# Kernel tuning notes

Measured on AMD Instinct MI355X. Metric: run time of the kernel, lower is better.

Reference implementation:

```python
import jax, jax.numpy as jnp
import numpy as np

N, E, B = 100000, 160000, 4096
F_NODE, F_EDGE, H, DEPTH = 133, 14, 512, 5


def setup_inputs() -> dict:
    key = jax.random.key(0)
    ks = jax.random.split(key, 12)
    P = E // 2
    src = jax.random.randint(ks[0], (P,), 0, N)
    dst = jax.random.randint(ks[1], (P,), 0, N)
    # interleave so edge 2k = (src,dst) and 2k+1 = (dst,src); reverse of e is e^1
    row = jnp.stack([src, dst], axis=1).reshape(-1)
    col = jnp.stack([dst, src], axis=1).reshape(-1)
    edge_index = jnp.stack([row, col], axis=0)
    x = jax.random.normal(ks[2], (N, F_NODE), jnp.float32)
    edge_attr = jax.random.normal(ks[3], (E, F_EDGE), jnp.float32)
    batch = jnp.sort(jax.random.randint(ks[4], (N,), 0, B))
    s = 0.05
    return dict(
        x=x, edge_attr=edge_attr, edge_index=edge_index, batch=batch,
        W_init=jax.random.normal(ks[5], (F_NODE + F_EDGE, H), jnp.float32) * s,
        b_init=jnp.zeros((H,), jnp.float32),
        W_conv=jax.random.normal(ks[6], (DEPTH, H, H), jnp.float32) * s,
        b_conv=jnp.zeros((DEPTH, H), jnp.float32),
        W_e2n=jax.random.normal(ks[7], (F_NODE + H, H), jnp.float32) * s,
        b_e2n=jnp.zeros((H,), jnp.float32),
        W_ffn1=jax.random.normal(ks[8], (H, H), jnp.float32) * s,
        b_ffn1=jnp.zeros((H,), jnp.float32),
        W_ffn2=jax.random.normal(ks[9], (H, 1), jnp.float32) * s,
        b_ffn2=jnp.zeros((1,), jnp.float32),
    )


def _dmpnn_conv(h, row, col, rev, W, b):
    # node aggregation: sum incoming edge messages at each destination node
    a = jax.ops.segment_sum(h, col, num_segments=N)          # [N, H]
    # new edge message for (i->j): agg at i minus reverse-edge message (j->i)
    msg = a[row] - h[rev]                                    # [E, H]
    return a, msg @ W + b


def reference(x, edge_attr, edge_index, batch, W_init, b_init, W_conv, b_conv,
              W_e2n, b_e2n, W_ffn1, b_ffn1, W_ffn2, b_ffn2):
    row, col = edge_index[0], edge_index[1]
    rev = jnp.arange(E) ^ 1
    # edge_init: relu(Linear(cat([x[row], edge_attr])))
    h0 = jax.nn.relu(jnp.concatenate([x[row], edge_attr], axis=1) @ W_init + b_init)
    h = h0
    for l in range(DEPTH):
        _, h = _dmpnn_conv(h, row, col, rev, W_conv[l], b_conv[l])
        h = jax.nn.relu(h + h0)  # residual to h0, relu (dropout=0, eval mode)
    # final conv reuses last layer (l == DEPTH-1 as in the torch loop variable)
    s_node, _ = _dmpnn_conv(h, row, col, rev, W_conv[DEPTH - 1], b_conv[DEPTH - 1])
    q = jnp.concatenate([x, s_node], axis=1)                 # [N, F_NODE+H]
    hn = jax.nn.relu(q @ W_e2n + b_e2n)                      # [N, H]
    pooled = jax.ops.segment_sum(hn, batch, num_segments=B)  # global_add_pool [B, H]
    out = jax.nn.relu(pooled @ W_ffn1 + b_ffn1) @ W_ffn2 + b_ffn2
    return out.squeeze(-1)                                   # [B]
```

## Files before the change

### kernel.cpp

```cpp
#include <hip/hip_runtime.h>

typedef _Float16 f16;
typedef _Float16 f16x2 __attribute__((ext_vector_type(2)));
typedef _Float16 f16x4 __attribute__((ext_vector_type(4)));
typedef _Float16 f16x8 __attribute__((ext_vector_type(8)));
typedef float f32x4 __attribute__((ext_vector_type(4)));

#define NN 100000
#define NE 160000
#define NB 4096
#define HD 512

#define O_H8    0UL
#define O_SCE   81920000UL
#define O_SHR   87040000UL
#define O_WT    141440000UL
#define O_OFF   145437696UL
#define O_EID   145837712UL
#define WS_NEEDED 146477712UL
#define V_POOL  0UL
#define V_PH    8388608UL
#define V_T1    12582912UL
#define V_CNT   16777216UL
#define V_FILL  17177232UL
#define V_BSUM  17577248UL

__global__ void zero16(ulong2* __restrict__ p, long n) {
  long i = (long)blockIdx.x * 256 + threadIdx.x;
  if (i < n) p[i] = ulong2{0UL, 0UL};
}
__global__ void diag(float* __restrict__ out, int n, float v) {
  int i = blockIdx.x * 256 + threadIdx.x;
  if (i < n) out[i] = v;
}

__global__ void transcast(const float* __restrict__ src, f16* __restrict__ dst,
                          int Kreal, int Kpad) {
  int id = blockIdx.x * 256 + threadIdx.x;
  if (id >= 512 * Kpad) return;
  int n = id / Kpad, k = id % Kpad;
  dst[((k >> 5) * 512 + n) * 32 + (k & 31)] =
      (k < Kreal) ? (f16)src[(size_t)k * 512 + n] : (f16)0.f;
}

__global__ void countK(const int* __restrict__ col, int* __restrict__ cnt) {
  int e = blockIdx.x * 256 + threadIdx.x;
  if (e < NE) atomicAdd(&cnt[col[e]], 1);
}
__global__ __launch_bounds__(1024) void scanA(const int* __restrict__ cnt,
                                              int* __restrict__ incl, int* __restrict__ bsum) {
  __shared__ int s[1024];
  int i = blockIdx.x * 1024 + threadIdx.x;
  s[threadIdx.x] = (i < NN) ? cnt[i] : 0;
  __syncthreads();
  for (int d = 1; d < 1024; d <<= 1) {
    int t = (threadIdx.x >= d) ? s[threadIdx.x - d] : 0;
    __syncthreads();
    s[threadIdx.x] += t;
    __syncthreads();
  }
  if (i < NN) incl[i] = s[threadIdx.x];
  if (threadIdx.x == 1023) bsum[blockIdx.x] = s[1023];
}
__global__ void scanB(int* bsum, int nb) {
  if (threadIdx.x == 0 && blockIdx.x == 0) {
    int run = 0;
    for (int i = 0; i < nb; ++i) { int t = bsum[i]; bsum[i] = run; run += t; }
  }
}
__global__ __launch_bounds__(1024) void scanC(const int* __restrict__ cnt,
                                              int* __restrict__ incl_fill,
                                              const int* __restrict__ bsum,
                                              int* __restrict__ off) {
  int i = blockIdx.x * 1024 + threadIdx.x;
  if (i >= NN) return;
  int g = incl_fill[i] + bsum[blockIdx.x];
  off[i + 1] = g;
  incl_fill[i] = g - cnt[i];
  if (i == 0) off[0] = 0;
}
__global__ void scatterK(const int* __restrict__ col, int* __restrict__ fill,
                         int* __restrict__ eid) {
  int e = blockIdx.x * 256 + threadIdx.x;
  if (e >= NE) return;
  int p = atomicAdd(&fill[col[e]], 1);
  eid[p] = e;
}

template<int C0>
__global__ __launch_bounds__(256, 4)
void msgk(const char* __restrict__ z8, const float* __restrict__ sce,
          const int* __restrict__ off, const int* __restrict__ eid,
          char* __restrict__ msgq, float* __restrict__ scm) {
  int tid = threadIdx.x, wid = tid >> 6, lane = tid & 63;
  int n = blockIdx.x * 4 + wid;
  int s0 = off[n], s1 = off[n + 1];
  int cnt = s1 - s0;
  int g = lane >> 4;
  float a[4] = {0.f, 0.f, 0.f, 0.f};
  int ec[8]; unsigned uc[8]; float scc[8];
  #pragma unroll
  for (int i = 0; i < 8; ++i) {
    if (i < cnt) {
      int e = eid[s0 + i];
      ec[i] = e;
      scc[i] = sce[e * 8 + (C0 >> 6) + g];
      uc[i] = *reinterpret_cast<const unsigned*>(z8 + (size_t)e * 512 + C0 + lane * 4);
      #pragma unroll
      for (int b = 0; b < 4; ++b)
        a[b] += (float)(char)((uc[i] >> (8 * b)) & 0xff) * scc[i];
    }
  }
  for (int p = s0 + 8; p < s1; ++p) {
    int e = eid[p];
    float sc = sce[e * 8 + (C0 >> 6) + g];
    unsigned u = *reinterpret_cast<const unsigned*>(z8 + (size_t)e * 512 + C0 + lane * 4);
    #pragma unroll
    for (int b = 0; b < 4; ++b)
      a[b] += (float)(char)((u >> (8 * b)) & 0xff) * sc;
  }
  #pragma unroll
  for (int i = 0; i < 8; ++i) {
    if (i < cnt) {
      int f = ec[i] ^ 1;
      float mv[4]; float m = 0.f;
      #pragma unroll
      for (int b = 0; b < 4; ++b) {
        mv[b] = a[b] - (float)(char)((uc[i] >> (8 * b)) & 0xff) * scc[i];
        m = fmaxf(m, fabsf(mv[b]));
      }
      #pragma unroll
      for (int d = 1; d < 16; d <<= 1) m = fmaxf(m, __shfl_xor(m, d));
      float s2 = (m > 0.f) ? m / 127.f : 1.f;
      if ((lane & 15) == 0) scm[f * 4 + g] = s2;
      unsigned q = 0;
      #pragma unroll
      for (int b = 0; b < 4; ++b) {
        int qi = __float2int_rn(mv[b] / s2);
        qi = min(127, max(-127, qi));
        q |= ((unsigned)(unsigned char)(char)qi) << (8 * b);
      }
      *reinterpret_cast<unsigned*>(msgq + (size_t)f * 256 + lane * 4) = q;
    }
  }
  for (int p = s0 + 8; p < s1; ++p) {
    int e = eid[p];
    int f = e ^ 1;
    float sc = sce[e * 8 + (C0 >> 6) + g];
    unsigned u = *reinterpret_cast<const unsigned*>(z8 + (size_t)e * 512 + C0 + lane * 4);
    float mv[4]; float m = 0.f;
    #pragma unroll
    for (int b = 0; b < 4; ++b) {
      mv[b] = a[b] - (float)(char)((u >> (8 * b)) & 0xff) * sc;
      m = fmaxf(m, fabsf(mv[b]));
    }
    #pragma unroll
    for (int d = 1; d < 16; d <<= 1) m = fmaxf(m, __shfl_xor(m, d));
    float s2 = (m > 0.f) ? m / 127.f : 1.f;
    if ((lane & 15) == 0) scm[f * 4 + g] = s2;
    unsigned q = 0;
    #pragma unroll
    for (int b = 0; b < 4; ++b) {
      int qi = __float2int_rn(mv[b] / s2);
      qi = min(127, max(-127, qi));
      q |= ((unsigned)(unsigned char)(char)qi) << (8 * b);
    }
    *reinterpret_cast<unsigned*>(msgq + (size_t)f * 256 + lane * 4) = q;
  }
}

__global__ __launch_bounds__(256, 4)
void tker(const char* __restrict__ h8, const float* __restrict__ sce,
          const int* __restrict__ off, const int* __restrict__ eid,
          char* __restrict__ nb8, float* __restrict__ scn) {
  int tid = threadIdx.x, wid = tid >> 6, lane = tid & 63;
  int n = blockIdx.x * 4 + wid;
  int s0 = off[n], s1 = off[n + 1];
  int g = lane >> 3;
  float a[8] = {0.f,0.f,0.f,0.f,0.f,0.f,0.f,0.f};
  for (int p = s0; p < s1; ++p) {
    int e = eid[p];
    float sc = sce[e * 8 + g];
    uint2 u = *reinterpret_cast<const uint2*>(h8 + (size_t)e * 512 + lane * 8);
    #pragma unroll
    for (int b = 0; b < 4; ++b) {
      a[b]     += (float)((u.x >> (8 * b)) & 0xff) * sc;
      a[4 + b] += (float)((u.y >> (8 * b)) & 0xff) * sc;
    }
  }
  float m = 0.f;
  #pragma unroll
  for (int j = 0; j < 8; ++j) m = fmaxf(m, a[j]);
  #pragma unroll
  for (int d = 1; d < 8; d <<= 1) m = fmaxf(m, __shfl_xor(m, d));
  float s2 = (m > 0.f) ? m / 255.f : 1.f;
  if ((lane & 7) == 0) scn[n * 8 + g] = s2;
  unsigned lo = 0, hi = 0;
  #pragma unroll
  for (int b = 0; b < 4; ++b) {
    int q0 = __float2int_rn(a[b] / s2);     q0 = min(255, max(0, q0));
    int q1 = __float2int_rn(a[4 + b] / s2); q1 = min(255, max(0, q1));
    lo |= ((unsigned)q0) << (8 * b);
    hi |= ((unsigned)q1) << (8 * b);
  }
  *reinterpret_cast<uint2*>(nb8 + (size_t)n * 512 + lane * 8) = uint2{lo, hi};
}

static __device__ __forceinline__ void stageB512(const f16* __restrict__ wsrc,
                                                 f16* __restrict__ Bs, int tid) {
  #pragma unroll
  for (int j = 0; j < 4; ++j) {
    int u = tid * 4 + j;
    *reinterpret_cast<f16x8*>(&Bs[(u >> 2) * 40 + (u & 3) * 8]) =
        *reinterpret_cast<const f16x8*>(&wsrc[u * 8]);
  }
}
template<int AS>
static __device__ __forceinline__ void mstep8(const f16* __restrict__ As,
                                              const f16* __restrict__ Bs,
                                              f32x4 acc[2][8], int wm, int wn,
                                              int fr, int fg, int ko) {
  f16x8 af[2];
  #pragma unroll
  for (int mf = 0; mf < 2; ++mf)
    af[mf] = *reinterpret_cast<const f16x8*>(&As[(wm + mf * 16 + fr) * AS + ko + fg * 8]);
  #pragma unroll
  for (int nf = 0; nf < 8; ++nf) {
    f16x8 bf = *reinterpret_cast<const f16x8*>(&Bs[(wn + nf * 16 + fr) * 40 + fg * 8]);
    #pragma unroll
    for (int mf = 0; mf < 2; ++mf)
      acc[mf][nf] = __builtin_amdgcn_mfma_f32_16x16x32_f16(af[mf], bf, acc[mf][nf], 0, 0, 0);
  }
}

static __device__ __forceinline__ void loadBfrag(const f16* __restrict__ wp,
                                                 f16x8 bf[8], int wn, int fr, int fg) {
  #pragma unroll
  for (int nf = 0; nf < 8; ++nf)
    bf[nf] = *reinterpret_cast<const f16x8*>(&wp[(size_t)(wn + nf * 16 + fr) * 32 + fg * 8]);
}

static __device__ __forceinline__ f16x2 pkfma(f16x2 a, f16x2 b, f16x2 c) {
  f16x2 r;
  asm("v_pk_fma_f16 %0, %1, %2, %3" : "=v"(r) : "v"(a), "v"(b), "v"(c));
  return r;
}

static __device__ __forceinline__ void stageXrow(const float* __restrict__ xr,
                                                 f16* __restrict__ dstRow, int s) {
  #pragma unroll
  for (int j = 0; j < 4; ++j) {
    float v[4];
    __builtin_memcpy(v, xr + 4 * s + 32 * j, 16);
    f16 t4[4];
    #pragma unroll
    for (int b = 0; b < 4; ++b) t4[b] = (f16)v[b];
    *reinterpret_cast<f16x4*>(&dstRow[4 * s + 32 * j]) = *reinterpret_cast<f16x4*>(t4);
  }
  if (s < 5) dstRow[128 + s] = (f16)xr[128 + s];
}

__global__ __launch_bounds__(512, 4)
void zk(char* __restrict__ h8, float* __restrict__ sce, const f16* __restrict__ wst) {
  __shared__ f16 Af[64 * 264];
  __shared__ f16 Bs[512 * 40];
  const int tid = threadIdx.x, lane = tid & 63, wid = tid >> 6;
  const int fr = lane & 15, fg = lane >> 4;
  const int wm = (wid >> 2) * 32, wn = (wid & 3) * 128;
  const int e0 = blockIdx.x * 64;
  const int sr = tid >> 3;
  const int sc8 = tid & 7;

  auto stageA = [&](int phase) {
    const int kb = phase * 256 + sc8 * 32;
    float sa = sce[(size_t)(e0 + sr) * 8 + (kb >> 6)];
    const f16 sh = (f16)sa;
    const f16 bh = (f16)(-1024.f * sa);
    f16x2 s2; s2[0] = sh; s2[1] = sh;
    f16x2 b2; b2[0] = bh; b2[1] = bh;
    const int4* src = reinterpret_cast<const int4*>(h8 + (size_t)(e0 + sr) * 512 + kb);
    f16* dst = &Af[sr * 264 + sc8 * 32];
    #pragma unroll
    for (int j = 0; j < 2; ++j) {
      int4 w = src[j];
      unsigned vv[4] = {(unsigned)w.x, (unsigned)w.y, (unsigned)w.z, (unsigned)w.w};
      #pragma unroll
      for (int q = 0; q < 2; ++q) {
        unsigned p0 = __builtin_amdgcn_perm(0x64646464u, vv[2*q],     0x05010400u);
        unsigned p1 = __builtin_amdgcn_perm(0x64646464u, vv[2*q],     0x05030402u);
        unsigned p2 = __builtin_amdgcn_perm(0x64646464u, vv[2*q + 1], 0x05010400u);
        unsigned p3 = __builtin_amdgcn_perm(0x64646464u, vv[2*q + 1], 0x05030402u);
        uint4 o;
        o.x = __builtin_bit_cast(unsigned, pkfma(__builtin_bit_cast(f16x2, p0), s2, b2));
        o.y = __builtin_bit_cast(unsigned, pkfma(__builtin_bit_cast(f16x2, p1), s2, b2));
        o.z = __builtin_bit_cast(unsigned, pkfma(__builtin_bit_cast(f16x2, p2), s2, b2));
        o.w = __builtin_bit_cast(unsigned, pkfma(__builtin_bit_cast(f16x2, p3), s2, b2));
        *reinterpret_cast<uint4*>(dst + j * 16 + q * 8) = o;
      }
    }
  };

  stageA(0);
  f32x4 acc[2][8] = {};
  for (int step = 0; step < 16; ++step) {
    if (step == 8) stageA(1);
    stageB512(wst + (size_t)step * 16384, Bs, tid);
    __syncthreads();
    const int ko = (step & 7) * 32;
    f16x8 af[2];
    #pragma unroll
    for (int mf = 0; mf < 2; ++mf)
      af[mf] = *reinterpret_cast<const f16x8*>(&Af[(wm + mf * 16 + fr) * 264 + ko + fg * 8]);
    #pragma unroll
    for (int nf = 0; nf < 8; ++nf) {
      f16x8 bf = *reinterpret_cast<const f16x8*>(&Bs[(wn + nf * 16 + fr) * 40 + fg * 8]);
      #pragma unroll
      for (int mf = 0; mf < 2; ++mf)
        acc[mf][nf] = __builtin_amdgcn_mfma_f32_16x16x32_f16(af[mf], bf, acc[mf][nf], 0, 0, 0);
    }
    __syncthreads();
  }
  float scA[2][4], scB[2][4];
  #pragma unroll
  for (int mf = 0; mf < 2; ++mf)
    #pragma unroll
    for (int i = 0; i < 4; ++i) {
      float mA = 0.f, mB = 0.f;
      #pragma unroll
      for (int nf = 0; nf < 4; ++nf) mA = fmaxf(mA, fabsf(acc[mf][nf][i]));
      #pragma unroll
      for (int nf = 4; nf < 8; ++nf) mB = fmaxf(mB, fabsf(acc[mf][nf][i]));
      #pragma unroll
      for (int d = 1; d < 16; d <<= 1) {
        mA = fmaxf(mA, __shfl_xor(mA, d));
        mB = fmaxf(mB, __shfl_xor(mB, d));
      }
      scA[mf][i] = (mA > 0.f) ? mA / 127.f : 1.f;
      scB[mf][i] = (mB > 0.f) ? mB / 127.f : 1.f;
      if (fr == 0) {
        int r = wm + mf * 16 + fg * 4 + i;
        sce[(size_t)(e0 + r) * 8 + (wn >> 6)]     = scA[mf][i];
        sce[(size_t)(e0 + r) * 8 + (wn >> 6) + 1] = scB[mf][i];
      }
    }
  char* q8 = (char*)&Bs[0];
  #pragma unroll
  for (int mf = 0; mf < 2; ++mf)
    #pragma unroll
    for (int nf = 0; nf < 8; ++nf) {
      int c = wn + nf * 16 + fr;
      #pragma unroll
      for (int i = 0; i < 4; ++i) {
        int r = wm + mf * 16 + fg * 4 + i;
        float s = (nf < 4) ? scA[mf][i] : scB[mf][i];
        int q = __float2int_rn(acc[mf][nf][i] / s);
        q8[r * 512 + c] = (char)min(127, max(-127, q));
      }
    }
  __syncthreads();
  { int4* dst = reinterpret_cast<int4*>(h8 + (size_t)e0 * 512);
    const int4* s4 = reinterpret_cast<const int4*>(q8);
    #pragma unroll
    for (int j = 0; j < 4; ++j) dst[tid * 4 + j] = s4[tid * 4 + j]; }
}

template<int MODE>
__global__ __launch_bounds__(512, 2)
void convup(const float* __restrict__ x, const float* __restrict__ ea,
            const int* __restrict__ row, const f16* __restrict__ wi,
            const float* __restrict__ bi, const float* __restrict__ bc,
            char* __restrict__ h8, float* __restrict__ sce,
            const char* __restrict__ msgq, const float* __restrict__ scm,
            int c0) {
  __shared__ f16 As[64 * 168];
  __shared__ f16 Bs[2][256 * 40];
  __shared__ char m8s[64 * 256];
  __shared__ float scmL[64 * 4];
  const int tid = threadIdx.x, lane = tid & 63, wid = tid >> 6;
  const int fr = lane & 15, fg = lane >> 4;
  const int wm = (wid >> 2) * 32, wn = (wid & 3) * 64;
  const int e0 = blockIdx.x * 64;

  {
    int r = tid >> 3, s = tid & 7;
    int rid = row[e0 + r];
    stageXrow(x + (size_t)rid * 133, &As[r * 168], s);
    if (s < 7) {
      float2 e2 = *reinterpret_cast<const float2*>(ea + (size_t)(e0 + r) * 14 + 2 * s);
      As[r * 168 + 133 + 2 * s]     = (f16)e2.x;
      As[r * 168 + 133 + 2 * s + 1] = (f16)e2.y;
    }
    for (int k = 147 + s; k < 160; k += 8) As[r * 168 + k] = (f16)0.f;
    if (MODE == 1) {
      const int4* ms = reinterpret_cast<const int4*>(msgq + (size_t)(e0 + r) * 256 + s * 32);
      int4* md = reinterpret_cast<int4*>(m8s + r * 256 + s * 32);
      md[0] = ms[0]; md[1] = ms[1];
      if (s < 4) scmL[r * 4 + s] = scm[(size_t)(e0 + r) * 4 + s];
    }
  }
  {
    #pragma unroll
    for (int j = 0; j < 2; ++j) {
      int u = tid * 2 + j;
      *reinterpret_cast<f16x8*>(&Bs[0][(u >> 2) * 40 + (u & 3) * 8]) =
          *reinterpret_cast<const f16x8*>(&wi[(size_t)c0 * 32 + (size_t)u * 8]);
    }
  }
  __syncthreads();
  f32x4 acc[2][4] = {};
  for (int step = 0; step < 5; ++step) {
    const int cur = step & 1;
    f16x8 pf[2];
    if (step < 4) {
      const f16* wsrc = wi + (size_t)(step + 1) * 16384 + (size_t)c0 * 32;
      #pragma unroll
      for (int j = 0; j < 2; ++j)
        pf[j] = *reinterpret_cast<const f16x8*>(&wsrc[(size_t)(tid * 2 + j) * 8]);
    }
    f16x8 af[2];
    #pragma unroll
    for (int mf = 0; mf < 2; ++mf)
      af[mf] = *reinterpret_cast<const f16x8*>(&As[(wm + mf * 16 + fr) * 168 + step * 32 + fg * 8]);
    #pragma unroll
    for (int nf = 0; nf < 4; ++nf) {
      f16x8 bf = *reinterpret_cast<const f16x8*>(&Bs[cur][(wn + nf * 16 + fr) * 40 + fg * 8]);
      #pragma unroll
      for (int mf = 0; mf < 2; ++mf)
        acc[mf][nf] = __builtin_amdgcn_mfma_f32_16x16x32_f16(af[mf], bf, acc[mf][nf], 0, 0, 0);
    }
    if (step < 4) {
      #pragma unroll
      for (int j = 0; j < 2; ++j) {
        int u = tid * 2 + j;
        *reinterpret_cast<f16x8*>(&Bs[cur ^ 1][(u >> 2) * 40 + (u & 3) * 8]) = pf[j];
      }
    }
    __syncthreads();
  }
  #pragma unroll
  for (int nf = 0; nf < 4; ++nf) {
    int cl = wn + nf * 16 + fr;
    int cg = c0 + cl;
    float bi_ = bi[cg];
    float bc_ = (MODE == 1) ? bc[cg] : 0.f;
    #pragma unroll
    for (int mf = 0; mf < 2; ++mf)
      #pragma unroll
      for (int i = 0; i < 4; ++i) {
        int r = wm + mf * 16 + fg * 4 + i;
        float v = fmaxf(acc[mf][nf][i] + bi_, 0.f);
        if (MODE == 1) {
          float mv = (float)(char)m8s[r * 256 + cl] * scmL[r * 4 + (cl >> 6)];
          v = fmaxf(v + bc_ + mv, 0.f);
        }
        acc[mf][nf][i] = v;
      }
  }
  float sc_[2][4];
  #pragma unroll
  for (int mf = 0; mf < 2; ++mf)
    #pragma unroll
    for (int i = 0; i < 4; ++i) {
      float m = 0.f;
      #pragma unroll
      for (int nf = 0; nf < 4; ++nf) m = fmaxf(m, acc[mf][nf][i]);
      #pragma unroll
      for (int d = 1; d < 16; d <<= 1) m = fmaxf(m, __shfl_xor(m, d));
      sc_[mf][i] = (m > 0.f) ? m / 255.f : 1.f;
      if (fr == 0)
        sce[(size_t)(e0 + wm + mf * 16 + fg * 4 + i) * 8 + (c0 >> 6) + (wn >> 6)] = sc_[mf][i];
    }
  __syncthreads();
  #pragma unroll
  for (int mf = 0; mf < 2; ++mf)
    #pragma unroll
    for (int nf = 0; nf < 4; ++nf) {
      int cl = wn + nf * 16 + fr;
      #pragma unroll
      for (int i = 0; i < 4; ++i) {
        int r = wm + mf * 16 + fg * 4 + i;
        int q = __float2int_rn(acc[mf][nf][i] / sc_[mf][i]);
        m8s[r * 256 + cl] = (char)(unsigned char)min(255, max(0, q));
      }
    }
  __syncthreads();
  { int r = tid >> 3, s = tid & 7;
    int4* dst = reinterpret_cast<int4*>(h8 + (size_t)(e0 + r) * 512 + c0 + s * 32);
    const int4* sp = reinterpret_cast<const int4*>(m8s + r * 256 + s * 32);
    dst[0] = sp[0]; dst[1] = sp[1]; }
}

__global__ __launch_bounds__(512, 4)
void e2n(const float* __restrict__ x, const char* __restrict__ nb8,
         const float* __restrict__ scn, const f16* __restrict__ wex,
         const f16* __restrict__ wes, const float* __restrict__ be,
         const int* __restrict__ batch, float* __restrict__ pooled) {
  __shared__ f16 As[64 * 520];
  __shared__ int bat[64];
  const int tid = threadIdx.x, lane = tid & 63, wid = tid >> 6;
  const int fr = lane & 15, fg = lane >> 4;
  const int wm = (wid >> 2) * 32, wn = (wid & 3) * 128;
  const int n0 = blockIdx.x * 64;
  if (tid < 64) { int nn = n0 + tid; bat[tid] = (nn < NN) ? batch[nn] : 0; }
  {
    int r = tid >> 3, s = tid & 7;
    int nid = min(n0 + r, NN - 1);
    stageXrow(x + (size_t)nid * 133, &As[r * 168], s);
    for (int k = 133 + s; k < 160; k += 8) As[r * 168 + k] = (f16)0.f;
  }
  __syncthreads();
  f32x4 acc[2][8] = {};
  for (int step = 0; step < 5; ++step) {
    f16x8 bf[8];
    loadBfrag(wex + (size_t)step * 16384, bf, wn, fr, fg);
    f16x8 af[2];
    #pragma unroll
    for (int mf = 0; mf < 2; ++mf)
      af[mf] = *reinterpret_cast<const f16x8*>(&As[(wm + mf * 16 + fr) * 168 + step * 32 + fg * 8]);
    #pragma unroll
    for (int nf = 0; nf < 8; ++nf)
      #pragma unroll
      for (int mf = 0; mf < 2; ++mf)
        acc[mf][nf] = __builtin_amdgcn_mfma_f32_16x16x32_f16(af[mf], bf[nf], acc[mf][nf], 0, 0, 0);
  }
  __syncthreads();
  {
    int r = tid >> 3, s = tid & 7, kb = s * 64;
    int nid = min(n0 + r, NN - 1);
    float sc = scn[(size_t)nid * 8 + s];
    const int4* src = reinterpret_cast<const int4*>(nb8 + (size_t)nid * 512 + kb);
    #pragma unroll
    for (int j = 0; j < 4; ++j) {
      int4 w = src[j];
      unsigned vv[4] = {(unsigned)w.x, (unsigned)w.y, (unsigned)w.z, (unsigned)w.w};
      f16 tmp[16];
      #pragma unroll
      for (int q = 0; q < 4; ++q)
        #pragma unroll
        for (int b = 0; b < 4; ++b)
          tmp[q * 4 + b] = (f16)((float)((vv[q] >> (8 * b)) & 0xff) * sc);
      *reinterpret_cast<f16x8*>(&As[r * 520 + kb + j * 16])     = *reinterpret_cast<f16x8*>(&tmp[0]);
      *reinterpret_cast<f16x8*>(&As[r * 520 + kb + j * 16 + 8]) = *reinterpret_cast<f16x8*>(&tmp[8]);
    }
  }
  __syncthreads();
  for (int step = 0; step < 16; ++step) {
    f16x8 bf[8];
    loadBfrag(wes + (size_t)step * 16384, bf, wn, fr, fg);
    f16x8 af[2];
    #pragma unroll
    for (int mf = 0; mf < 2; ++mf)
      af[mf] = *reinterpret_cast<const f16x8*>(&As[(wm + mf * 16 + fr) * 520 + step * 32 + fg * 8]);
    #pragma unroll
    for (int nf = 0; nf < 8; ++nf)
      #pragma unroll
      for (int mf = 0; mf < 2; ++mf)
        acc[mf][nf] = __builtin_amdgcn_mfma_f32_16x16x32_f16(af[mf], bf[nf], acc[mf][nf], 0, 0, 0);
  }
  __syncthreads();
  #pragma unroll
  for (int nf = 0; nf < 8; ++nf) {
    int c = wn + nf * 16 + fr;
    float b_ = be[c];
    #pragma unroll
    for (int mf = 0; mf < 2; ++mf)
      #pragma unroll
      for (int i = 0; i < 4; ++i) {
        int rl = wm + mf * 16 + fg * 4 + i;
        As[rl * 520 + c] = (f16)fmaxf(acc[mf][nf][i] + b_, 0.f);
      }
  }
  __syncthreads();
  {
    const int c = tid;
    float s = 0.f;
    int pb = bat[0];
    #pragma unroll 1
    for (int r = 0; r < 64; ++r) {
      if (n0 + r >= NN) break;
      int b = bat[r];
      if (b != pb) {
        atomicAdd(&pooled[(size_t)pb * 512 + c], s);
        s = 0.f; pb = b;
      }
      s += (float)As[r * 520 + c];
    }
    atomicAdd(&pooled[(size_t)pb * 512 + c], s);
  }
}

__global__ __launch_bounds__(512, 1)
void ffn1(const f16* __restrict__ ph, const f16* __restrict__ wf,
          const float* __restrict__ b1, f16* __restrict__ t1) {
  __shared__ f16 As[64 * 520];
  __shared__ f16 Bs[2][512 * 40];
  const int tid = threadIdx.x, lane = tid & 63, wid = tid >> 6;
  const int fr = lane & 15, fg = lane >> 4;
  const int wm = (wid >> 2) * 32, wn = (wid & 3) * 128;
  const int n0 = blockIdx.x * 64;
  { int r = tid >> 3, hs = (tid & 7) * 64;
    #pragma unroll
    for (int j = 0; j < 8; ++j)
      *reinterpret_cast<f16x8*>(&As[r * 520 + hs + j * 8]) =
          *reinterpret_cast<const f16x8*>(&ph[(size_t)(n0 + r) * 512 + hs + j * 8]); }
  stageB512(wf, Bs[0], tid);
  __syncthreads();
  f32x4 acc[2][8] = {};
  for (int step = 0; step < 16; ++step) {
    const int cur = step & 1;
    f16x8 pf[4];
    if (step < 15) {
      const f16* wsrc = wf + (size_t)(step + 1) * 16384;
      #pragma unroll
      for (int j = 0; j < 4; ++j)
        pf[j] = *reinterpret_cast<const f16x8*>(&wsrc[(size_t)(tid * 4 + j) * 8]);
    }
    mstep8<520>(As, Bs[cur], acc, wm, wn, fr, fg, step * 32);
    if (step < 15) {
      #pragma unroll
      for (int j = 0; j < 4; ++j) {
        int u = tid * 4 + j;
        *reinterpret_cast<f16x8*>(&Bs[cur ^ 1][(u >> 2) * 40 + (u & 3) * 8]) = pf[j];
      }
    }
    __syncthreads();
  }
  f16* q16 = As;
  #pragma unroll
  for (int nf = 0; nf < 8; ++nf) {
    int c = wn + nf * 16 + fr;
    float b_ = b1[c];
    #pragma unroll
    for (int mf = 0; mf < 2; ++mf)
      #pragma unroll
      for (int i = 0; i < 4; ++i) {
        int r = wm + mf * 16 + fg * 4 + i;
        q16[r * 512 + c] = (f16)fmaxf(acc[mf][nf][i] + b_, 0.f);
      }
  }
  __syncthreads();
  #pragma unroll
  for (int j = 0; j < 8; ++j)
    *reinterpret_cast<f16x8*>(&t1[(size_t)n0 * 512 + tid * 64 + j * 8]) =
        *reinterpret_cast<const f16x8*>(&q16[tid * 64 + j * 8]);
}

__global__ void cast_ph(const float* __restrict__ pooled, f16* __restrict__ ph) {
  int id = blockIdx.x * 256 + threadIdx.x;
  if (id >= NB * 64) return;
  int k = id * 8;
  f16 v[8];
  #pragma unroll
  for (int i = 0; i < 8; ++i) v[i] = (f16)pooled[k + i];
  *reinterpret_cast<f16x8*>(&ph[k]) = *reinterpret_cast<f16x8*>(&v[0]);
}

__global__ void final_out(const f16* __restrict__ t, const float* __restrict__ W2,
                          const float* __restrict__ b2, float* __restrict__ out) {
  int id = blockIdx.x * 256 + threadIdx.x;
  if (id >= NB * 64) return;
  int b = id >> 6, lane = id & 63;
  f16x8 v = *reinterpret_cast<const f16x8*>(&t[(size_t)b * HD + lane * 8]);
  float s = 0.f;
  #pragma unroll
  for (int i = 0; i < 8; ++i) s += (float)v[i] * W2[lane * 8 + i];
  #pragma unroll
  for (int o = 32; o > 0; o >>= 1) s += __shfl_down(s, o);
  if (lane == 0) out[b] = s + b2[0];
}

extern "C" void kernel_launch(void* const* d_in, const int* in_sizes, int n_in,
                              void* d_out, int out_size, void* d_ws, size_t ws_size,
                              hipStream_t stream) {
  const float* x      = (const float*)d_in[0];
  const float* ea     = (const float*)d_in[1];
  const int*   ei     = (const int*)d_in[2];
  const int*   batch  = (const int*)d_in[3];
  const float* W_init = (const float*)d_in[4];
  const float* b_init = (const float*)d_in[5];
  const float* W_conv = (const float*)d_in[6];
  const float* b_conv = (const float*)d_in[7];
  const float* W_e2n  = (const float*)d_in[8];
  const float* b_e2n  = (const float*)d_in[9];
  const float* W_ffn1 = (const float*)d_in[10];
  const float* b_ffn1 = (const float*)d_in[11];
  const float* W_ffn2 = (const float*)d_in[12];
  const float* b_ffn2 = (const float*)d_in[13];
  const int* row = ei;
  const int* col = ei + NE;
  float* out = (float*)d_out;

  if (ws_size < WS_NEEDED) {
    diag<<<(out_size + 255) / 256, 256, 0, stream>>>(out, out_size, (float)(ws_size >> 20));
    return;
  }

  char* ws = (char*)d_ws;
  char*  h8   = ws + O_H8;
  float* sce  = (float*)(ws + O_SCE);
  char*  msgq = ws + O_SHR;
  float* scm  = (float*)(ws + O_SHR + 40960000UL);
  char*  nb8  = ws + O_SHR;
  float* scn  = (float*)(ws + O_SHR + 51200000UL);
  f16*   wt   = (f16*)(ws + O_WT);
  int*   off  = (int*)(ws + O_OFF);
  int*   eid  = (int*)(ws + O_EID);
  float* pooled = (float*)(ws + V_POOL);
  f16*   ph   = (f16*)(ws + V_PH);
  f16*   t1   = (f16*)(ws + V_T1);
  int*   cnt  = (int*)(ws + V_CNT);
  int*   fill = (int*)(ws + V_FILL);
  int*   bsum = (int*)(ws + V_BSUM);

  f16* wi  = wt;
  f16* wc  = wi + 160 * 512;
  f16* wex = wc + 5 * 512 * 512;
  f16* wes = wex + 160 * 512;
  f16* wf1 = wes + 512 * 512;

  transcast<<<(512 * 160 + 255) / 256, 256, 0, stream>>>(W_init, wi, 147, 160);
  for (int l = 0; l < 5; ++l)
    transcast<<<(512 * 512 + 255) / 256, 256, 0, stream>>>(
        W_conv + (size_t)l * 262144, wc + (size_t)l * 262144, 512, 512);
  transcast<<<(512 * 160 + 255) / 256, 256, 0, stream>>>(W_e2n, wex, 133, 160);
  transcast<<<(512 * 512 + 255) / 256, 256, 0, stream>>>(W_e2n + 133 * 512, wes, 512, 512);
  transcast<<<(512 * 512 + 255) / 256, 256, 0, stream>>>(W_ffn1, wf1, 512, 512);

  zero16<<<(25000 + 255) / 256, 256, 0, stream>>>((ulong2*)cnt, 25000);
  countK<<<(NE + 255) / 256, 256, 0, stream>>>(col, cnt);
  scanA<<<98, 1024, 0, stream>>>(cnt, fill, bsum);
  scanB<<<1, 64, 0, stream>>>(bsum, 98);
  scanC<<<98, 1024, 0, stream>>>(cnt, fill, bsum, off);
  scatterK<<<(NE + 255) / 256, 256, 0, stream>>>(col, fill, eid);

  convup<0><<<2500, 512, 0, stream>>>(x, ea, row, wi, b_init, nullptr,
                                      h8, sce, nullptr, nullptr, 0);
  convup<0><<<2500, 512, 0, stream>>>(x, ea, row, wi, b_init, nullptr,
                                      h8, sce, nullptr, nullptr, 256);
  for (int l = 0; l < 5; ++l) {
    zk<<<2500, 512, 0, stream>>>(h8, sce, wc + (size_t)l * 262144);
    msgk<0><<<25000, 256, 0, stream>>>(h8, sce, off, eid, msgq, scm);
    convup<1><<<2500, 512, 0, stream>>>(x, ea, row, wi, b_init, b_conv + l * 512,
                                        h8, sce, msgq, scm, 0);
    msgk<256><<<25000, 256, 0, stream>>>(h8, sce, off, eid, msgq, scm);
    convup<1><<<2500, 512, 0, stream>>>(x, ea, row, wi, b_init, b_conv + l * 512,
                                        h8, sce, msgq, scm, 256);
  }
  tker<<<25000, 256, 0, stream>>>(h8, sce, off, eid, nb8, scn);
  zero16<<<(524288 + 255) / 256, 256, 0, stream>>>((ulong2*)pooled, 524288);
  e2n<<<1563, 512, 0, stream>>>(x, nb8, scn, wex, wes, b_e2n, batch, pooled);
  cast_ph<<<(NB * 64 + 255) / 256, 256, 0, stream>>>(pooled, ph);
  ffn1<<<64, 512, 0, stream>>>(ph, wf1, b_ffn1, t1);
  final_out<<<(NB * 64 + 255) / 256, 256, 0, stream>>>(t1, W_ffn2, b_ffn2, out);
}
```

Before: 2.437 ms.

## Restructure zk GEMM into 32-row blocks with per-wave register-prefetched weight tiles

The zk kernel moves from 64-edge blocks of 512 threads to 32-edge blocks of 256 threads, each wave owning a 128-column slice. Each wave stages its own B tile in a private LDS buffer and prefetches the next step's weights into registers while the MFMAs run, so the per-step block-wide barriers go away. The aim is to overlap weight loads with compute and drop synchronisation. In exchange, every block now reads the full weight matrix for only half as many rows, which doubles weight traffic, and register pressure goes up.

```diff
diff --git a/kernel.cpp b/kernel.cpp
--- a/kernel.cpp
+++ b/kernel.cpp
@@ -260,14 +260,14 @@
   if (s < 5) dstRow[128 + s] = (f16)xr[128 + s];
 }
 
-__global__ __launch_bounds__(512, 4)
+__global__ __launch_bounds__(256, 2)
 void zk(char* __restrict__ h8, float* __restrict__ sce, const f16* __restrict__ wst) {
-  __shared__ f16 Af[64 * 264];
-  __shared__ f16 Bs[512 * 40];
+  __shared__ f16 Af[32 * 264];
+  __shared__ f16 Bw[4][128 * 40];
   const int tid = threadIdx.x, lane = tid & 63, wid = tid >> 6;
   const int fr = lane & 15, fg = lane >> 4;
-  const int wm = (wid >> 2) * 32, wn = (wid & 3) * 128;
-  const int e0 = blockIdx.x * 64;
+  const int wn = wid * 128;
+  const int e0 = blockIdx.x * 32;
   const int sr = tid >> 3;
   const int sc8 = tid & 7;
 
@@ -300,26 +300,45 @@
     }
   };
 
+  auto stageBw = [&](int s, f16x8* pf) {
+    const f16* wsrc = wst + (size_t)s * 16384 + (size_t)wn * 32;
+    #pragma unroll
+    for (int j = 0; j < 8; ++j)
+      pf[j] = *reinterpret_cast<const f16x8*>(&wsrc[(size_t)(j * 64 + lane) * 8]);
+  };
+  auto writeBw = [&](f16x8* pf) {
+    #pragma unroll
+    for (int j = 0; j < 8; ++j) {
+      int u = j * 64 + lane;
+      *reinterpret_cast<f16x8*>(&Bw[wid][(u >> 2) * 40 + (u & 3) * 8]) = pf[j];
+    }
+  };
+
   stageA(0);
+  { f16x8 p0[8]; stageBw(0, p0); writeBw(p0); }
+  __syncthreads();
   f32x4 acc[2][8] = {};
   for (int step = 0; step < 16; ++step) {
-    if (step == 8) stageA(1);
-    stageB512(wst + (size_t)step * 16384, Bs, tid);
-    __syncthreads();
+    if (step == 8) { __syncthreads(); stageA(1); __syncthreads(); }
+    f16x8 pf[8];
+    if (step < 15) stageBw(step + 1, pf);
     const int ko = (step & 7) * 32;
     f16x8 af[2];
     #pragma unroll
     for (int mf = 0; mf < 2; ++mf)
-      af[mf] = *reinterpret_cast<const f16x8*>(&Af[(wm + mf * 16 + fr) * 264 + ko + fg * 8]);
-    #pragma unroll
-    for (int nf = 0; nf < 8; ++nf) {
-      f16x8 bf = *reinterpret_cast<const f16x8*>(&Bs[(wn + nf * 16 + fr) * 40 + fg * 8]);
+      af[mf] = *reinterpret_cast<const f16x8*>(&Af[(mf * 16 + fr) * 264 + ko + fg * 8]);
+    f16x8 bf[8];
+    #pragma unroll
+    for (int nf = 0; nf < 8; ++nf)
+      bf[nf] = *reinterpret_cast<const f16x8*>(&Bw[wid][(nf * 16 + fr) * 40 + fg * 8]);
+    #pragma unroll
+    for (int nf = 0; nf < 8; ++nf)
       #pragma unroll
       for (int mf = 0; mf < 2; ++mf)
-        acc[mf][nf] = __builtin_amdgcn_mfma_f32_16x16x32_f16(af[mf], bf, acc[mf][nf], 0, 0, 0);
-    }
-    __syncthreads();
-  }
+        acc[mf][nf] = __builtin_amdgcn_mfma_f32_16x16x32_f16(af[mf], bf[nf], acc[mf][nf], 0, 0, 0);
+    if (step < 15) writeBw(pf);
+  }
+  __syncthreads();
   float scA[2][4], scB[2][4];
   #pragma unroll
   for (int mf = 0; mf < 2; ++mf)
@@ -338,12 +357,12 @@
       scA[mf][i] = (mA > 0.f) ? mA / 127.f : 1.f;
       scB[mf][i] = (mB > 0.f) ? mB / 127.f : 1.f;
       if (fr == 0) {
-        int r = wm + mf * 16 + fg * 4 + i;
+        int r = mf * 16 + fg * 4 + i;
         sce[(size_t)(e0 + r) * 8 + (wn >> 6)]     = scA[mf][i];
         sce[(size_t)(e0 + r) * 8 + (wn >> 6) + 1] = scB[mf][i];
       }
     }
-  char* q8 = (char*)&Bs[0];
+  char* q8 = (char*)&Bw[0][0];
   #pragma unroll
   for (int mf = 0; mf < 2; ++mf)
     #pragma unroll
@@ -351,17 +370,18 @@
       int c = wn + nf * 16 + fr;
       #pragma unroll
       for (int i = 0; i < 4; ++i) {
-        int r = wm + mf * 16 + fg * 4 + i;
+        int r = mf * 16 + fg * 4 + i;
         float s = (nf < 4) ? scA[mf][i] : scB[mf][i];
         int q = __float2int_rn(acc[mf][nf][i] / s);
         q8[r * 512 + c] = (char)min(127, max(-127, q));
       }
     }
   __syncthreads();
-  { int4* dst = reinterpret_cast<int4*>(h8 + (size_t)e0 * 512);
-    const int4* s4 = reinterpret_cast<const int4*>(q8);
-    #pragma unroll
-    for (int j = 0; j < 4; ++j) dst[tid * 4 + j] = s4[tid * 4 + j]; }
+  { int r = tid >> 3, kb = (tid & 7) * 64;
+    int4* dst = reinterpret_cast<int4*>(h8 + (size_t)(e0 + r) * 512 + kb);
+    const int4* s4 = reinterpret_cast<const int4*>(&q8[r * 512 + kb]);
+    #pragma unroll
+    for (int j = 0; j < 4; ++j) dst[j] = s4[j]; }
 }
 
 template<int MODE>
@@ -738,7 +758,7 @@
   convup<0><<<2500, 512, 0, stream>>>(x, ea, row, wi, b_init, nullptr,
                                       h8, sce, nullptr, nullptr, 256);
   for (int l = 0; l < 5; ++l) {
-    zk<<<2500, 512, 0, stream>>>(h8, sce, wc + (size_t)l * 262144);
+    zk<<<5000, 256, 0, stream>>>(h8, sce, wc + (size_t)l * 262144);
     msgk<0><<<25000, 256, 0, stream>>>(h8, sce, off, eid, msgq, scm);
     convup<1><<<2500, 512, 0, stream>>>(x, ea, row, wi, b_init, b_conv + l * 512,
                                         h8, sce, msgq, scm, 0);
```

Result: slower. 2.617 ms (+7.4%).
